# Kernel optimization log

Hardware: AMD Instinct MI355X
Metric: run time of the kernel (lower is better)

## Reference

```python
import jax, jax.numpy as jnp
import numpy as np

B, T, D, U = 64, 2048, 512, 512

def setup_inputs() -> dict:
    key = jax.random.key(0)
    ks = jax.random.split(key, 5)
    scale = 1.0 / np.sqrt(D)
    return {
        "query": jax.random.normal(ks[0], (B, D), dtype=jnp.float32),
        "values": jax.random.normal(ks[1], (B, T, D), dtype=jnp.float32),
        "W1": jax.random.normal(ks[2], (D, U), dtype=jnp.float32) * scale,
        "b1": jnp.zeros((U,), dtype=jnp.float32),
        "W2": jax.random.normal(ks[3], (D, U), dtype=jnp.float32) * scale,
        "b2": jnp.zeros((U,), dtype=jnp.float32),
        "Wv": jax.random.normal(ks[4], (U, 1), dtype=jnp.float32) * (1.0 / np.sqrt(U)),
        "bv": jnp.zeros((1,), dtype=jnp.float32),
    }

def reference(query, values, W1, b1, W2, b2, Wv, bv):
    # mask: True where the timestep has any nonzero feature -> [B, T, 1]
    mask = ~jnp.all(values == 0, axis=-1, keepdims=True)
    # query gets a broadcast time axis: [B, 1, U]
    q_proj = query @ W1 + b1                       # [B, U]
    v_proj = jnp.einsum('btd,du->btu', values, W2) + b2  # [B, T, U]
    hidden = jnp.tanh(q_proj[:, None, :] + v_proj)       # [B, T, U]
    score = hidden @ Wv + bv                       # [B, T, 1]
    score = jnp.where(mask, score, -jnp.inf)
    attention_weights = jax.nn.softmax(score, axis=1)    # [B, T, 1]
    # matmul(attn^T, values) -> [B, 1, D]; reduce_sum over axis=1 -> [B, D]
    context_vector = jnp.einsum('bt,btd->bd', attention_weights[..., 0], values)
    return context_vector, attention_weights
```

## Files before the change

### kernel.cpp

```cpp
#include <hip/hip_runtime.h>
#include <hip/hip_bf16.h>
#include <math.h>

#define B_ 64
#define T_ 2048
#define D_ 512
#define U_ 512

typedef __attribute__((ext_vector_type(8))) short short8;
typedef __attribute__((ext_vector_type(4))) float f32x4;

__device__ __forceinline__ unsigned int f2bf(float x) {
  unsigned int u = __float_as_uint(x);
  unsigned int r = u + 0x7fffu + ((u >> 16) & 1u);
  return r >> 16;
}

__device__ __forceinline__ float tanh_fast(float x) {
  float e = __expf(2.f * x);
  return 1.f - 2.f * __builtin_amdgcn_rcpf(e + 1.f);
}

__device__ __forceinline__ unsigned swz4(unsigned rc) { return (rc + (rc >> 2)) & 3u; }

__global__ __launch_bounds__(256) void k_qproj(const float* __restrict__ query,
                                               const float* __restrict__ W1,
                                               const float* __restrict__ b1,
                                               float* __restrict__ qproj) {
  const int b = blockIdx.x;
  const int tid = threadIdx.x;
  __shared__ float q[D_];
  q[tid] = query[b * D_ + tid];
  q[tid + 256] = query[b * D_ + tid + 256];
  __syncthreads();
  float a0 = 0.f, a1 = 0.f;
#pragma unroll 8
  for (int d = 0; d < D_; d++) {
    float qd = q[d];
    a0 = fmaf(qd, W1[d * U_ + tid], a0);
    a1 = fmaf(qd, W1[d * U_ + tid + 256], a1);
  }
  qproj[b * U_ + tid] = a0 + b1[tid];
  qproj[b * U_ + tid + 256] = a1 + b1[tid + 256];
}

__global__ __launch_bounds__(256) void k_w2t(const float* __restrict__ W2,
                                             unsigned short* __restrict__ w2t) {
  __shared__ float tile[32][33];
  const int k0 = blockIdx.y * 32, u0 = blockIdx.x * 32;
  const int tx = threadIdx.x, ty = threadIdx.y;
#pragma unroll
  for (int r = 0; r < 4; r++)
    tile[ty + 8 * r][tx] = W2[(size_t)(k0 + ty + 8 * r) * U_ + (u0 + tx)];
  __syncthreads();
#pragma unroll
  for (int r = 0; r < 4; r++) {
    int u_l = ty + 8 * r, k_l = tx;
    w2t[(size_t)(u0 + u_l) * D_ + (k0 + k_l)] = (unsigned short)f2bf(tile[k_l][u_l]);
  }
}

__device__ __forceinline__ void storeA(char* bufA, float4 av, unsigned awoff,
                                       int* rowflag, int arow) {
  if (av.x != 0.f || av.y != 0.f || av.z != 0.f || av.w != 0.f) rowflag[arow] = 1;
  uint2 pk;
  pk.x = f2bf(av.x) | (f2bf(av.y) << 16);
  pk.y = f2bf(av.z) | (f2bf(av.w) << 16);
  *(uint2*)(bufA + awoff) = pk;
}

__global__ __launch_bounds__(512, 4) void k_score(
    const float* __restrict__ values, const unsigned short* __restrict__ w2t,
    const float* __restrict__ qproj, const float* __restrict__ b2,
    const float* __restrict__ Wv, const float* __restrict__ bv,
    float* __restrict__ scores) {
  __shared__ __align__(16) unsigned short lsA[2][64 * 32];
  __shared__ __align__(16) unsigned short lsB[2][512 * 32];
  __shared__ float qp[U_];
  __shared__ float wv_s[U_];
  __shared__ float red[64 * 8];
  __shared__ int rowflag[64];

  const int tid = threadIdx.x;
  const int wid = tid >> 6;
  const int lane = tid & 63;
  const int m0 = blockIdx.x * 64;
  const int b = m0 >> 11;

  qp[tid] = qproj[b * U_ + tid] + b2[tid];
  wv_s[tid] = Wv[tid];
  if (tid < 64) rowflag[tid] = 0;

  const int arow = tid >> 3;
  const int achunk = tid & 7;
  const float* aptr = values + (size_t)(m0 + arow) * D_ + achunk * 4;
  const unsigned awoff = (unsigned)(arow * 64) +
                         ((((unsigned)achunk >> 1) ^ swz4((unsigned)arow)) << 4) +
                         ((unsigned)(achunk & 1) << 3);

  const int bcol0 = tid >> 2;
  const unsigned bs = (unsigned)(tid & 3);

  char* lsAc = (char*)lsA;
  char* lsBc = (char*)lsB;
  const int colbase = wid * 64;

  f32x4 acc[4][4];
#pragma unroll
  for (int i = 0; i < 4; i++)
#pragma unroll
    for (int j = 0; j < 4; j++) acc[i][j] = (f32x4){0.f, 0.f, 0.f, 0.f};

  asm volatile("s_waitcnt vmcnt(0)" ::: "memory");

  float4 av = *(const float4*)aptr;
  asm volatile("" ::: "memory");
#pragma unroll
  for (int r = 0; r < 4; r++) {
    int col = bcol0 + r * 128;
    const unsigned short* src = w2t + (size_t)col * D_ + ((bs ^ swz4((unsigned)col)) << 3);
    __builtin_amdgcn_global_load_lds(
        (const __attribute__((address_space(1))) unsigned int*)src,
        (__attribute__((address_space(3))) unsigned int*)(lsBc + wid * 1024 + r * 8192),
        16, 0, 0);
  }
  asm volatile("s_waitcnt vmcnt(4)" ::: "memory");
  storeA(lsAc, av, awoff, rowflag, arow);
  asm volatile("s_waitcnt lgkmcnt(0)" ::: "memory");
  __builtin_amdgcn_s_barrier();

#pragma unroll 1
  for (int t = 0; t < 15; t++) {
    char* curA = lsAc + (t & 1) * 4096;
    char* curB = lsBc + (t & 1) * 32768;
    char* nxtA = lsAc + ((t + 1) & 1) * 4096;
    char* nxtB = lsBc + ((t + 1) & 1) * 32768;
    const int kk = (t + 1) * 32;

    float4 av2 = *(const float4*)(aptr + kk);
    asm volatile("" ::: "memory");
#pragma unroll
    for (int r = 0; r < 4; r++) {
      int col = bcol0 + r * 128;
      const unsigned short* src =
          w2t + (size_t)col * D_ + kk + ((bs ^ swz4((unsigned)col)) << 3);
      __builtin_amdgcn_global_load_lds(
          (const __attribute__((address_space(1))) unsigned int*)src,
          (__attribute__((address_space(3))) unsigned int*)(nxtB + wid * 1024 + r * 8192),
          16, 0, 0);
    }
    asm volatile("s_waitcnt vmcnt(5)" ::: "memory");

    short8 af[4], bf[4];
#pragma unroll
    for (int fr = 0; fr < 4; fr++) {
      int row = fr * 16 + (lane & 15);
      af[fr] = *(const short8*)(curA + row * 64 +
                                ((((unsigned)lane >> 4) ^ swz4((unsigned)row)) << 4));
    }
#pragma unroll
    for (int fc = 0; fc < 4; fc++) {
      int col = colbase + fc * 16 + (lane & 15);
      bf[fc] = *(const short8*)(curB + col * 64 +
                                ((((unsigned)lane >> 4) ^ swz4((unsigned)col)) << 4));
    }
#pragma unroll
    for (int fr = 0; fr < 4; fr++)
#pragma unroll
      for (int fc = 0; fc < 4; fc++)
        acc[fr][fc] = __builtin_amdgcn_mfma_f32_16x16x32_bf16(af[fr], bf[fc], acc[fr][fc], 0, 0, 0);

    asm volatile("s_waitcnt vmcnt(4)" ::: "memory");
    storeA(nxtA, av2, awoff, rowflag, arow);
    asm volatile("s_waitcnt lgkmcnt(0)" ::: "memory");
    __builtin_amdgcn_s_barrier();
  }

  asm volatile("s_waitcnt vmcnt(0)" ::: "memory");
  {
    char* curA = lsAc + 4096;
    char* curB = lsBc + 32768;
    short8 af[4], bf[4];
#pragma unroll
    for (int fr = 0; fr < 4; fr++) {
      int row = fr * 16 + (lane & 15);
      af[fr] = *(const short8*)(curA + row * 64 +
                                ((((unsigned)lane >> 4) ^ swz4((unsigned)row)) << 4));
    }
#pragma unroll
    for (int fc = 0; fc < 4; fc++) {
      int col = colbase + fc * 16 + (lane & 15);
      bf[fc] = *(const short8*)(curB + col * 64 +
                                ((((unsigned)lane >> 4) ^ swz4((unsigned)col)) << 4));
    }
#pragma unroll
    for (int fr = 0; fr < 4; fr++)
#pragma unroll
      for (int fc = 0; fc < 4; fc++)
        acc[fr][fc] = __builtin_amdgcn_mfma_f32_16x16x32_bf16(af[fr], bf[fc], acc[fr][fc], 0, 0, 0);
  }

  const int rgrp = lane >> 4;
  const int cl = lane & 15;
  float ps[4][4];
#pragma unroll
  for (int fr = 0; fr < 4; fr++)
#pragma unroll
    for (int r = 0; r < 4; r++) ps[fr][r] = 0.f;

#pragma unroll
  for (int fc = 0; fc < 4; fc++) {
    int u = colbase + fc * 16 + cl;
    float qpu = qp[u], wvu = wv_s[u];
#pragma unroll
    for (int fr = 0; fr < 4; fr++)
#pragma unroll
      for (int r = 0; r < 4; r++)
        ps[fr][r] = fmaf(tanh_fast(acc[fr][fc][r] + qpu), wvu, ps[fr][r]);
  }
#pragma unroll
  for (int fr = 0; fr < 4; fr++)
#pragma unroll
    for (int r = 0; r < 4; r++) {
      float v = ps[fr][r];
      v += __shfl_xor(v, 1, 64);
      v += __shfl_xor(v, 2, 64);
      v += __shfl_xor(v, 4, 64);
      v += __shfl_xor(v, 8, 64);
      if (cl == 0) red[(fr * 16 + rgrp * 4 + r) * 8 + wid] = v;
    }
  __syncthreads();
  if (tid < 64) {
    float s = bv[0];
#pragma unroll
    for (int w = 0; w < 8; w++) s += red[tid * 8 + w];
    if (!rowflag[tid]) s = -INFINITY;
    scores[m0 + tid] = s;
  }
}

__global__ __launch_bounds__(256) void k_softmax(const float* __restrict__ scores,
                                                 float* __restrict__ attn) {
  const int b = blockIdx.x, tid = threadIdx.x;
  const float* srow = scores + (size_t)b * T_;
  float s[8];
  float m = -INFINITY;
#pragma unroll
  for (int j = 0; j < 8; j++) {
    s[j] = srow[tid + 256 * j];
    m = fmaxf(m, s[j]);
  }
#pragma unroll
  for (int o = 1; o < 64; o <<= 1) m = fmaxf(m, __shfl_xor(m, o, 64));
  __shared__ float redm[4], redsum[4];
  if ((tid & 63) == 0) redm[tid >> 6] = m;
  __syncthreads();
  m = fmaxf(fmaxf(redm[0], redm[1]), fmaxf(redm[2], redm[3]));
  float sum = 0.f;
#pragma unroll
  for (int j = 0; j < 8; j++) {
    s[j] = __expf(s[j] - m);
    sum += s[j];
  }
#pragma unroll
  for (int o = 1; o < 64; o <<= 1) sum += __shfl_xor(sum, o, 64);
  if ((tid & 63) == 0) redsum[tid >> 6] = sum;
  __syncthreads();
  sum = redsum[0] + redsum[1] + redsum[2] + redsum[3];
  float inv = 1.f / sum;
#pragma unroll
  for (int j = 0; j < 8; j++) attn[(size_t)b * T_ + tid + 256 * j] = s[j] * inv;
}

__global__ __launch_bounds__(128) void k_ctx_part(const float* __restrict__ values,
                                                  const float* __restrict__ attn,
                                                  float* __restrict__ part) {
  const int tc = blockIdx.x, b = blockIdx.y;
  const int tid = threadIdx.x;
  const float4* vp = (const float4*)(values + ((size_t)b * T_ + tc * 128) * D_);
  const float* ap = attn + (size_t)b * T_ + tc * 128;
  float4 acc = {0.f, 0.f, 0.f, 0.f};
#pragma unroll 4
  for (int t = 0; t < 128; t++) {
    float w = ap[t];
    float4 v = vp[(size_t)t * 128 + tid];
    acc.x = fmaf(w, v.x, acc.x);
    acc.y = fmaf(w, v.y, acc.y);
    acc.z = fmaf(w, v.z, acc.z);
    acc.w = fmaf(w, v.w, acc.w);
  }
  float4* pp = (float4*)(part + (size_t)(b * 16 + tc) * D_);
  pp[tid] = acc;
}

__global__ __launch_bounds__(256) void k_ctx_reduce(const float* __restrict__ part,
                                                    float* __restrict__ ctx) {
  const int gid = blockIdx.x * 256 + threadIdx.x;
  const int b = gid >> 9, d = gid & 511;
  float s = 0.f;
#pragma unroll
  for (int tc = 0; tc < 16; tc++) s += part[(size_t)(b * 16 + tc) * D_ + d];
  ctx[gid] = s;
}

extern "C" void kernel_launch(void* const* d_in, const int* in_sizes, int n_in,
                              void* d_out, int out_size, void* d_ws, size_t ws_size,
                              hipStream_t stream) {
  const float* query  = (const float*)d_in[0];
  const float* values = (const float*)d_in[1];
  const float* W1     = (const float*)d_in[2];
  const float* b1     = (const float*)d_in[3];
  const float* W2     = (const float*)d_in[4];
  const float* b2     = (const float*)d_in[5];
  const float* Wv     = (const float*)d_in[6];
  const float* bv     = (const float*)d_in[7];

  float* out_ctx = (float*)d_out;
  float* out_attn = out_ctx + B_ * D_;

  char* ws = (char*)d_ws;
  float* qproj          = (float*)ws;
  unsigned short* w2t   = (unsigned short*)(ws + (128 << 10));
  float* scores         = (float*)(ws + (640 << 10));
  float* part           = (float*)(ws + (1152 << 10));

  k_qproj<<<dim3(B_), dim3(256), 0, stream>>>(query, W1, b1, qproj);
  k_w2t<<<dim3(16, 16), dim3(32, 8), 0, stream>>>(W2, w2t);
  k_score<<<dim3((B_ * T_) / 64), dim3(512), 0, stream>>>(values, w2t, qproj, b2, Wv, bv, scores);
  k_softmax<<<dim3(B_), dim3(256), 0, stream>>>(scores, out_attn);
  k_ctx_part<<<dim3(16, B_), dim3(128), 0, stream>>>(values, out_attn, part);
  k_ctx_reduce<<<dim3(128), dim3(256), 0, stream>>>(part, out_ctx);
}
```

Before: 207.6 us.

## Deepen k_score prefetch to two stages and restructure B tile loading

Restructures the score GEMM main loop so global loads for step t+2 are issued right after the compute barrier, overlapping two k-steps of loads with MFMA work instead of one. B-tile loads are reassigned so each wave fetches contiguous 16-column groups with a simpler XOR swizzle. Row-nonzero flags are now kept in registers and reduced by shuffle at the end, not written to shared memory every step. Shared memory is packed into one pool. The cost is more in-flight registers and more complex vmcnt bookkeeping, which is easy to get wrong.

```diff
diff --git a/kernel.cpp b/kernel.cpp
--- a/kernel.cpp
+++ b/kernel.cpp
@@ -20,8 +20,6 @@
   float e = __expf(2.f * x);
   return 1.f - 2.f * __builtin_amdgcn_rcpf(e + 1.f);
 }
-
-__device__ __forceinline__ unsigned swz4(unsigned rc) { return (rc + (rc >> 2)) & 3u; }
 
 __global__ __launch_bounds__(256) void k_qproj(const float* __restrict__ query,
                                                const float* __restrict__ W1,
@@ -60,50 +58,40 @@
   }
 }
 
-__device__ __forceinline__ void storeA(char* bufA, float4 av, unsigned awoff,
-                                       int* rowflag, int arow) {
-  if (av.x != 0.f || av.y != 0.f || av.z != 0.f || av.w != 0.f) rowflag[arow] = 1;
-  uint2 pk;
-  pk.x = f2bf(av.x) | (f2bf(av.y) << 16);
-  pk.y = f2bf(av.z) | (f2bf(av.w) << 16);
-  *(uint2*)(bufA + awoff) = pk;
-}
-
 __global__ __launch_bounds__(512, 4) void k_score(
     const float* __restrict__ values, const unsigned short* __restrict__ w2t,
     const float* __restrict__ qproj, const float* __restrict__ b2,
     const float* __restrict__ Wv, const float* __restrict__ bv,
     float* __restrict__ scores) {
-  __shared__ __align__(16) unsigned short lsA[2][64 * 32];
-  __shared__ __align__(16) unsigned short lsB[2][512 * 32];
-  __shared__ float qp[U_];
-  __shared__ float wv_s[U_];
-  __shared__ float red[64 * 8];
-  __shared__ int rowflag[64];
+  __shared__ __align__(16) char pool[80128];
+  char* lsA = pool;
+  char* lsB = pool + 8192;
+  float* qp = (float*)(pool + 73728);
+  float* wv_s = (float*)(pool + 75776);
+  float* red = (float*)(pool + 77824);
+  int* flg = (int*)(pool + 79872);
 
   const int tid = threadIdx.x;
   const int wid = tid >> 6;
   const int lane = tid & 63;
+  const int cl = lane & 15;
+  const int kg = lane >> 4;
   const int m0 = blockIdx.x * 64;
   const int b = m0 >> 11;
 
   qp[tid] = qproj[b * U_ + tid] + b2[tid];
   wv_s[tid] = Wv[tid];
-  if (tid < 64) rowflag[tid] = 0;
+  const float bv0 = bv[0];
 
   const int arow = tid >> 3;
-  const int achunk = tid & 7;
-  const float* aptr = values + (size_t)(m0 + arow) * D_ + achunk * 4;
+  const int akq = tid & 7;
+  const float* aptr = values + (size_t)(m0 + arow) * D_ + akq * 4;
   const unsigned awoff = (unsigned)(arow * 64) +
-                         ((((unsigned)achunk >> 1) ^ swz4((unsigned)arow)) << 4) +
-                         ((unsigned)(achunk & 1) << 3);
-
-  const int bcol0 = tid >> 2;
-  const unsigned bs = (unsigned)(tid & 3);
-
-  char* lsAc = (char*)lsA;
-  char* lsBc = (char*)lsB;
-  const int colbase = wid * 64;
+                         ((unsigned)(((akq >> 1) ^ ((arow >> 1) & 3)) & 3) << 4) +
+                         ((unsigned)(akq & 1) << 3);
+
+  const int bcol = (lane >> 2);
+  const int bslot = (lane & 3);
 
   f32x4 acc[4][4];
 #pragma unroll
@@ -111,58 +99,64 @@
 #pragma unroll
     for (int j = 0; j < 4; j++) acc[i][j] = (f32x4){0.f, 0.f, 0.f, 0.f};
 
+  int rf = 0;
+
   asm volatile("s_waitcnt vmcnt(0)" ::: "memory");
 
-  float4 av = *(const float4*)aptr;
-  asm volatile("" ::: "memory");
+  float4 aC, aN;
+  aC = *(const float4*)aptr;
 #pragma unroll
   for (int r = 0; r < 4; r++) {
-    int col = bcol0 + r * 128;
-    const unsigned short* src = w2t + (size_t)col * D_ + ((bs ^ swz4((unsigned)col)) << 3);
+    int ii = wid * 4 + r;
+    int col = ii * 16 + bcol;
+    int s = bslot ^ ((col >> 1) & 3);
+    const unsigned short* src = w2t + (size_t)col * D_ + s * 8;
     __builtin_amdgcn_global_load_lds(
         (const __attribute__((address_space(1))) unsigned int*)src,
-        (__attribute__((address_space(3))) unsigned int*)(lsBc + wid * 1024 + r * 8192),
+        (__attribute__((address_space(3))) unsigned int*)(lsB + ii * 1024),
         16, 0, 0);
   }
-  asm volatile("s_waitcnt vmcnt(4)" ::: "memory");
-  storeA(lsAc, av, awoff, rowflag, arow);
+  aN = *(const float4*)(aptr + 32);
+#pragma unroll
+  for (int r = 0; r < 4; r++) {
+    int ii = wid * 4 + r;
+    int col = ii * 16 + bcol;
+    int s = bslot ^ ((col >> 1) & 3);
+    const unsigned short* src = w2t + (size_t)col * D_ + 32 + s * 8;
+    __builtin_amdgcn_global_load_lds(
+        (const __attribute__((address_space(1))) unsigned int*)src,
+        (__attribute__((address_space(3))) unsigned int*)(lsB + 32768 + ii * 1024),
+        16, 0, 0);
+  }
+  asm volatile("s_waitcnt vmcnt(9)" ::: "memory");
+  {
+    if (aC.x != 0.f || aC.y != 0.f || aC.z != 0.f || aC.w != 0.f) rf = 1;
+    uint2 pk;
+    pk.x = f2bf(aC.x) | (f2bf(aC.y) << 16);
+    pk.y = f2bf(aC.z) | (f2bf(aC.w) << 16);
+    *(uint2*)(lsA + awoff) = pk;
+  }
+  asm volatile("s_waitcnt vmcnt(5)" ::: "memory");
   asm volatile("s_waitcnt lgkmcnt(0)" ::: "memory");
   __builtin_amdgcn_s_barrier();
+  aC = aN;
 
 #pragma unroll 1
-  for (int t = 0; t < 15; t++) {
-    char* curA = lsAc + (t & 1) * 4096;
-    char* curB = lsBc + (t & 1) * 32768;
-    char* nxtA = lsAc + ((t + 1) & 1) * 4096;
-    char* nxtB = lsBc + ((t + 1) & 1) * 32768;
-    const int kk = (t + 1) * 32;
-
-    float4 av2 = *(const float4*)(aptr + kk);
-    asm volatile("" ::: "memory");
-#pragma unroll
-    for (int r = 0; r < 4; r++) {
-      int col = bcol0 + r * 128;
-      const unsigned short* src =
-          w2t + (size_t)col * D_ + kk + ((bs ^ swz4((unsigned)col)) << 3);
-      __builtin_amdgcn_global_load_lds(
-          (const __attribute__((address_space(1))) unsigned int*)src,
-          (__attribute__((address_space(3))) unsigned int*)(nxtB + wid * 1024 + r * 8192),
-          16, 0, 0);
-    }
-    asm volatile("s_waitcnt vmcnt(5)" ::: "memory");
+  for (int t = 0; t < 16; t++) {
+    char* curA = lsA + (t & 1) * 4096;
+    char* curB = lsB + (t & 1) * 32768;
+    char* nxtA = lsA + ((t + 1) & 1) * 4096;
 
     short8 af[4], bf[4];
 #pragma unroll
     for (int fr = 0; fr < 4; fr++) {
-      int row = fr * 16 + (lane & 15);
-      af[fr] = *(const short8*)(curA + row * 64 +
-                                ((((unsigned)lane >> 4) ^ swz4((unsigned)row)) << 4));
+      int row = fr * 16 + cl;
+      af[fr] = *(const short8*)(curA + row * 64 + (((kg ^ ((row >> 1) & 3)) & 3) << 4));
     }
 #pragma unroll
     for (int fc = 0; fc < 4; fc++) {
-      int col = colbase + fc * 16 + (lane & 15);
-      bf[fc] = *(const short8*)(curB + col * 64 +
-                                ((((unsigned)lane >> 4) ^ swz4((unsigned)col)) << 4));
+      int col = wid * 64 + fc * 16 + cl;
+      bf[fc] = *(const short8*)(curB + col * 64 + (((kg ^ ((col >> 1) & 3)) & 3) << 4));
     }
 #pragma unroll
     for (int fr = 0; fr < 4; fr++)
@@ -170,47 +164,60 @@
       for (int fc = 0; fc < 4; fc++)
         acc[fr][fc] = __builtin_amdgcn_mfma_f32_16x16x32_bf16(af[fr], bf[fc], acc[fr][fc], 0, 0, 0);
 
-    asm volatile("s_waitcnt vmcnt(4)" ::: "memory");
-    storeA(nxtA, av2, awoff, rowflag, arow);
-    asm volatile("s_waitcnt lgkmcnt(0)" ::: "memory");
     __builtin_amdgcn_s_barrier();
-  }
-
-  asm volatile("s_waitcnt vmcnt(0)" ::: "memory");
-  {
-    char* curA = lsAc + 4096;
-    char* curB = lsBc + 32768;
-    short8 af[4], bf[4];
-#pragma unroll
-    for (int fr = 0; fr < 4; fr++) {
-      int row = fr * 16 + (lane & 15);
-      af[fr] = *(const short8*)(curA + row * 64 +
-                                ((((unsigned)lane >> 4) ^ swz4((unsigned)row)) << 4));
-    }
-#pragma unroll
-    for (int fc = 0; fc < 4; fc++) {
-      int col = colbase + fc * 16 + (lane & 15);
-      bf[fc] = *(const short8*)(curB + col * 64 +
-                                ((((unsigned)lane >> 4) ^ swz4((unsigned)col)) << 4));
-    }
-#pragma unroll
-    for (int fr = 0; fr < 4; fr++)
-#pragma unroll
-      for (int fc = 0; fc < 4; fc++)
-        acc[fr][fc] = __builtin_amdgcn_mfma_f32_16x16x32_bf16(af[fr], bf[fc], acc[fr][fc], 0, 0, 0);
-  }
+    asm volatile("" ::: "memory");
+
+    if (t < 14) {
+      const int kk = (t + 2) * 32;
+      aN = *(const float4*)(aptr + kk);
+#pragma unroll
+      for (int r = 0; r < 4; r++) {
+        int ii = wid * 4 + r;
+        int col = ii * 16 + bcol;
+        int s = bslot ^ ((col >> 1) & 3);
+        const unsigned short* src = w2t + (size_t)col * D_ + kk + s * 8;
+        __builtin_amdgcn_global_load_lds(
+            (const __attribute__((address_space(1))) unsigned int*)src,
+            (__attribute__((address_space(3))) unsigned int*)(curB + ii * 1024),
+            16, 0, 0);
+      }
+    }
+    if (t < 15) {
+      if (t < 14) {
+        asm volatile("s_waitcnt vmcnt(9)" ::: "memory");
+      } else {
+        asm volatile("s_waitcnt vmcnt(4)" ::: "memory");
+      }
+      if (aC.x != 0.f || aC.y != 0.f || aC.z != 0.f || aC.w != 0.f) rf = 1;
+      uint2 pk;
+      pk.x = f2bf(aC.x) | (f2bf(aC.y) << 16);
+      pk.y = f2bf(aC.z) | (f2bf(aC.w) << 16);
+      *(uint2*)(nxtA + awoff) = pk;
+      if (t < 14) {
+        asm volatile("s_waitcnt vmcnt(5)" ::: "memory");
+      } else {
+        asm volatile("s_waitcnt vmcnt(0)" ::: "memory");
+      }
+      asm volatile("s_waitcnt lgkmcnt(0)" ::: "memory");
+      __builtin_amdgcn_s_barrier();
+      aC = aN;
+    }
+  }
+
+  rf |= __shfl_xor(rf, 1, 64);
+  rf |= __shfl_xor(rf, 2, 64);
+  rf |= __shfl_xor(rf, 4, 64);
+  if ((tid & 7) == 0) flg[arow] = rf;
 
   const int rgrp = lane >> 4;
-  const int cl = lane & 15;
   float ps[4][4];
 #pragma unroll
   for (int fr = 0; fr < 4; fr++)
 #pragma unroll
     for (int r = 0; r < 4; r++) ps[fr][r] = 0.f;
-
 #pragma unroll
   for (int fc = 0; fc < 4; fc++) {
-    int u = colbase + fc * 16 + cl;
+    int u = wid * 64 + fc * 16 + cl;
     float qpu = qp[u], wvu = wv_s[u];
 #pragma unroll
     for (int fr = 0; fr < 4; fr++)
@@ -231,10 +238,10 @@
     }
   __syncthreads();
   if (tid < 64) {
-    float s = bv[0];
+    float s = bv0;
 #pragma unroll
     for (int w = 0; w < 8; w++) s += red[tid * 8 + w];
-    if (!rowflag[tid]) s = -INFINITY;
+    if (!flg[tid]) s = -INFINITY;
     scores[m0 + tid] = s;
   }
 }
```

Result: no change. 209.6 us (+0.9%).
